# Performance work log

Hardware: AMD Instinct MI355X
Metric: run time of the kernel (lower is better)

Reference implementation:

```python
import jax, jax.numpy as jnp
import numpy as np

S, B, C = 14, 2, 20          # grid size, boxes per cell, classes
LAMBDA_COORD, LAMBDA_NOOBJ = 5.0, 0.5
NCH = 5 * B + C              # 30 channels


def setup_inputs() -> dict:
    key = jax.random.key(0)
    k1, k2, k3 = jax.random.split(key, 3)
    Nb = 4096
    # positive values: loss takes sqrt(w), sqrt(h)
    pred = jax.random.uniform(k1, (Nb, S, S, NCH), dtype=jnp.float32, minval=0.05, maxval=1.0)
    target = jax.random.uniform(k2, (Nb, S, S, NCH), dtype=jnp.float32, minval=0.05, maxval=1.0)
    # binarize conf channels so coord (conf>0) / noobj (conf==0) partition the cells
    objf = (jax.random.uniform(k3, (Nb, S, S)) < 0.3).astype(jnp.float32)
    for b in range(B):
        target = target.at[..., 4 + 5 * b].set(objf)
    return {"pred_tensor": pred, "target_tensor": target}


def _to_xyxy(box):
    # box [..., 5] (or [..., B, 5]): cell-relative x,y and global w,h -> corners
    xy = box[..., :2] / S
    half = 0.5 * box[..., 2:4]
    return jnp.concatenate([xy - half, xy + half], axis=-1)


def reference(pred_tensor, target_tensor):
    pred, target = pred_tensor, target_tensor
    obj = (target[..., 4] > 0).astype(pred.dtype)      # [Nb,S,S]
    noobj = (target[..., 4] == 0).astype(pred.dtype)   # [Nb,S,S]

    pb = pred[..., :5 * B].reshape(pred.shape[:3] + (B, 5))     # [Nb,S,S,B,5]
    tb = target[..., :5 * B].reshape(target.shape[:3] + (B, 5))  # [Nb,S,S,B,5]

    # no-object confidence loss: conf channel of every box slot in noobj cells
    loss_noobj = jnp.sum(noobj[..., None] * (pb[..., 4] - tb[..., 4]) ** 2)

    # IoU of each of B predicted boxes vs the (first) target box of the cell
    pxy = _to_xyxy(pb)                        # [Nb,S,S,B,4]
    txy = _to_xyxy(tb[..., 0, :])[..., None, :]  # [Nb,S,S,1,4]
    lt = jnp.maximum(pxy[..., :2], txy[..., :2])
    rb = jnp.minimum(pxy[..., 2:], txy[..., 2:])
    wh = jnp.clip(rb - lt, 0.0)
    inter = wh[..., 0] * wh[..., 1]           # [Nb,S,S,B]
    area_p = (pxy[..., 2] - pxy[..., 0]) * (pxy[..., 3] - pxy[..., 1])
    area_t = (txy[..., 2] - txy[..., 0]) * (txy[..., 3] - txy[..., 1])
    iou = inter / (area_p + area_t - inter)

    max_iou = jax.lax.stop_gradient(jnp.max(iou, axis=-1))  # torch uses .data (detach)
    r = jnp.argmax(iou, axis=-1)              # responsible box index [Nb,S,S]

    pr = jnp.take_along_axis(pb, r[..., None, None], axis=3)[..., 0, :]  # [Nb,S,S,5]
    tr = jnp.take_along_axis(tb, r[..., None, None], axis=3)[..., 0, :]

    m = obj
    loss_xy = jnp.sum(m[..., None] * (pr[..., :2] - tr[..., :2]) ** 2)
    # guard sqrt in masked-out cells (values there don't matter)
    safe_pwh = jnp.where(m[..., None] > 0, pr[..., 2:4], 1.0)
    safe_twh = jnp.where(m[..., None] > 0, tr[..., 2:4], 1.0)
    loss_wh = jnp.sum(m[..., None] * (jnp.sqrt(safe_pwh) - jnp.sqrt(safe_twh)) ** 2)
    loss_obj = jnp.sum(m * (pr[..., 4] - max_iou) ** 2)
    loss_class = jnp.sum(m[..., None] * (pred[..., 5 * B:] - target[..., 5 * B:]) ** 2)

    loss = LAMBDA_COORD * (loss_xy + loss_wh) + loss_obj + LAMBDA_NOOBJ * loss_noobj + loss_class
    return loss / pred.shape[0]
```

## Files before the change

kernel.cpp:

```cpp
#include <hip/hip_runtime.h>


#define S_GRID 14
#define NB 4096
#define NCELL (NB * S_GRID * S_GRID)
#define NCH 30
#define CELLS_PER_BLOCK 256
#define NBLOCKS (NCELL / CELLS_PER_BLOCK)
#define FLOATS_PER_BLOCK (CELLS_PER_BLOCK * NCH)

#define GLOBAL_AS __attribute__((address_space(1)))
#define LDS_AS    __attribute__((address_space(3)))

__device__ __forceinline__ void async_copy16(const float* g, float* l) {
    __builtin_amdgcn_global_load_lds((const GLOBAL_AS void*)g, (LDS_AS void*)l,
                                     16, 0, 0);
}

__global__ __launch_bounds__(256) void yolo_loss_partial(
    const float* __restrict__ pred, const float* __restrict__ target,
    float* __restrict__ partial)
{
    __shared__ float ps[FLOATS_PER_BLOCK];
    __shared__ float ts[FLOATS_PER_BLOCK];

    const int tid = threadIdx.x;
    const size_t base = (size_t)blockIdx.x * FLOATS_PER_BLOCK;

#pragma unroll
    for (int r = 0; r < 8; ++r) {
        int idx = r * 256 + tid;
        if (idx < FLOATS_PER_BLOCK / 4) {
            async_copy16(pred + base + (size_t)idx * 4, ps + idx * 4);
            async_copy16(target + base + (size_t)idx * 4, ts + idx * 4);
        }
    }
    __syncthreads();

    float loss;
    {
        float p[NCH], t[NCH];
        const float2* p2 = (const float2*)(ps + tid * NCH);
        const float2* t2 = (const float2*)(ts + tid * NCH);
#pragma unroll
        for (int i = 0; i < NCH / 2; ++i) {
            float2 a = p2[i]; p[2 * i] = a.x; p[2 * i + 1] = a.y;
            float2 b = t2[i]; t[2 * i] = b.x; t[2 * i + 1] = b.y;
        }

        const float t4 = t[4];
        const bool obj = (t4 > 0.0f);

        float dn0 = p[4] - t[4];
        float dn1 = p[9] - t[9];
        float noobj_l = (t4 == 0.0f) ? (dn0 * dn0 + dn1 * dn1) : 0.0f;

        const float invS = 1.0f / 14.0f;
        float tcx = t[0] * invS, tcy = t[1] * invS;
        float tx1 = tcx - 0.5f * t[2], ty1 = tcy - 0.5f * t[3];
        float tx2 = tcx + 0.5f * t[2], ty2 = tcy + 0.5f * t[3];
        float area_t = (tx2 - tx1) * (ty2 - ty1);

        float iou[2];
#pragma unroll
        for (int b = 0; b < 2; ++b) {
            const float* pb = p + 5 * b;
            float cx = pb[0] * invS, cy = pb[1] * invS;
            float x1 = cx - 0.5f * pb[2], y1 = cy - 0.5f * pb[3];
            float x2 = cx + 0.5f * pb[2], y2 = cy + 0.5f * pb[3];
            float lx = fmaxf(x1, tx1), ly = fmaxf(y1, ty1);
            float rx = fminf(x2, tx2), ry = fminf(y2, ty2);
            float wx = fmaxf(rx - lx, 0.0f), wy = fmaxf(ry - ly, 0.0f);
            float inter = wx * wy;
            float area_p = (x2 - x1) * (y2 - y1);
            iou[b] = inter / (area_p + area_t - inter);
        }

        int r = (iou[1] > iou[0]) ? 1 : 0;
        float max_iou = fmaxf(iou[0], iou[1]);

        float obj_l = 0.0f;
        if (obj) {
            const float* pr = p + 5 * r;
            const float* tr = t + 5 * r;
            float dx = pr[0] - tr[0], dy = pr[1] - tr[1];
            float lxy = dx * dx + dy * dy;
            float dw = sqrtf(pr[2]) - sqrtf(tr[2]);
            float dh = sqrtf(pr[3]) - sqrtf(tr[3]);
            float lwh = dw * dw + dh * dh;
            float dob = pr[4] - max_iou;
            float lob = dob * dob;
            float lcls = 0.0f;
#pragma unroll
            for (int c = 10; c < 30; ++c) {
                float d = p[c] - t[c];
                lcls += d * d;
            }
            obj_l = 5.0f * (lxy + lwh) + lob + lcls;
        }
        loss = obj_l + 0.5f * noobj_l;
    }

    float v = loss;
#pragma unroll
    for (int off = 32; off > 0; off >>= 1)
        v += __shfl_down(v, off, 64);

    __shared__ float red[4];
    const int lane = threadIdx.x & 63;
    const int wid = threadIdx.x >> 6;
    if (lane == 0) red[wid] = v;
    __syncthreads();
    if (threadIdx.x == 0)
        partial[blockIdx.x] = red[0] + red[1] + red[2] + red[3];
}

__global__ __launch_bounds__(256) void yolo_loss_finalize(
    const float* __restrict__ partial, float* __restrict__ out)
{
    double s = 0.0;
    for (int i = threadIdx.x; i < NBLOCKS; i += 256)
        s += (double)partial[i];

    __shared__ double sh[256];
    sh[threadIdx.x] = s;
    __syncthreads();
#pragma unroll
    for (int step = 128; step > 0; step >>= 1) {
        if (threadIdx.x < step) sh[threadIdx.x] += sh[threadIdx.x + step];
        __syncthreads();
    }
    if (threadIdx.x == 0)
        out[0] = (float)(sh[0] / (double)NB);
}

extern "C" void kernel_launch(void* const* d_in, const int* in_sizes, int n_in,
                              void* d_out, int out_size, void* d_ws, size_t ws_size,
                              hipStream_t stream) {
    const float* pred = (const float*)d_in[0];
    const float* target = (const float*)d_in[1];
    float* out = (float*)d_out;
    float* partial = (float*)d_ws;

    yolo_loss_partial<<<NBLOCKS, 256, 0, stream>>>(pred, target, partial);
    yolo_loss_finalize<<<1, 256, 0, stream>>>(partial, out);
}
```

Before: 207.1 us.

## Load cell data directly from global memory instead of staging through LDS

Drops the async global-to-LDS staging of each block's pred and target tiles and the barrier after it. Each thread now reads its own cell's 30 floats straight from global memory as float2 loads, and the class loss is computed unconditionally. Launch bounds are raised to request 4 blocks per CU, since about 61 KB of LDS per block no longer limits occupancy. The trade-off is that per-thread strided 120-byte loads are poorly coalesced compared with the contiguous 16-byte staged copies, so more memory transactions may be issued.

```diff
diff --git a/kernel.cpp b/kernel.cpp
--- a/kernel.cpp
+++ b/kernel.cpp
@@ -7,99 +7,76 @@
 #define NCH 30
 #define CELLS_PER_BLOCK 256
 #define NBLOCKS (NCELL / CELLS_PER_BLOCK)
-#define FLOATS_PER_BLOCK (CELLS_PER_BLOCK * NCH)
 
-#define GLOBAL_AS __attribute__((address_space(1)))
-#define LDS_AS    __attribute__((address_space(3)))
-
-__device__ __forceinline__ void async_copy16(const float* g, float* l) {
-    __builtin_amdgcn_global_load_lds((const GLOBAL_AS void*)g, (LDS_AS void*)l,
-                                     16, 0, 0);
-}
-
-__global__ __launch_bounds__(256) void yolo_loss_partial(
+__global__ __launch_bounds__(256, 4) void yolo_loss_partial(
     const float* __restrict__ pred, const float* __restrict__ target,
     float* __restrict__ partial)
 {
-    __shared__ float ps[FLOATS_PER_BLOCK];
-    __shared__ float ts[FLOATS_PER_BLOCK];
+    const int cell = blockIdx.x * CELLS_PER_BLOCK + threadIdx.x;
+    const float2* __restrict__ p2 = (const float2*)(pred + (size_t)cell * NCH);
+    const float2* __restrict__ t2 = (const float2*)(target + (size_t)cell * NCH);
 
-    const int tid = threadIdx.x;
-    const size_t base = (size_t)blockIdx.x * FLOATS_PER_BLOCK;
+    float p[10], t[10];
+#pragma unroll
+    for (int i = 0; i < 5; ++i) {
+        float2 a = p2[i]; p[2 * i] = a.x; p[2 * i + 1] = a.y;
+        float2 b = t2[i]; t[2 * i] = b.x; t[2 * i + 1] = b.y;
+    }
 
+    const float t4 = t[4];
+    const bool obj = (t4 > 0.0f);
+
+    float dn0 = p[4] - t[4];
+    float dn1 = p[9] - t[9];
+    float noobj_l = (t4 == 0.0f) ? (dn0 * dn0 + dn1 * dn1) : 0.0f;
+
+    const float invS = 1.0f / 14.0f;
+    float tcx = t[0] * invS, tcy = t[1] * invS;
+    float tx1 = tcx - 0.5f * t[2], ty1 = tcy - 0.5f * t[3];
+    float tx2 = tcx + 0.5f * t[2], ty2 = tcy + 0.5f * t[3];
+    float area_t = (tx2 - tx1) * (ty2 - ty1);
+
+    float iou[2];
 #pragma unroll
-    for (int r = 0; r < 8; ++r) {
-        int idx = r * 256 + tid;
-        if (idx < FLOATS_PER_BLOCK / 4) {
-            async_copy16(pred + base + (size_t)idx * 4, ps + idx * 4);
-            async_copy16(target + base + (size_t)idx * 4, ts + idx * 4);
-        }
+    for (int b = 0; b < 2; ++b) {
+        const float* pb = p + 5 * b;
+        float cx = pb[0] * invS, cy = pb[1] * invS;
+        float x1 = cx - 0.5f * pb[2], y1 = cy - 0.5f * pb[3];
+        float x2 = cx + 0.5f * pb[2], y2 = cy + 0.5f * pb[3];
+        float lx = fmaxf(x1, tx1), ly = fmaxf(y1, ty1);
+        float rx = fminf(x2, tx2), ry = fminf(y2, ty2);
+        float wx = fmaxf(rx - lx, 0.0f), wy = fmaxf(ry - ly, 0.0f);
+        float inter = wx * wy;
+        float area_p = (x2 - x1) * (y2 - y1);
+        iou[b] = inter / (area_p + area_t - inter);
     }
-    __syncthreads();
 
-    float loss;
-    {
-        float p[NCH], t[NCH];
-        const float2* p2 = (const float2*)(ps + tid * NCH);
-        const float2* t2 = (const float2*)(ts + tid * NCH);
+    int r = (iou[1] > iou[0]) ? 1 : 0;
+    float max_iou = fmaxf(iou[0], iou[1]);
+
+    float lcls = 0.0f;
 #pragma unroll
-        for (int i = 0; i < NCH / 2; ++i) {
-            float2 a = p2[i]; p[2 * i] = a.x; p[2 * i + 1] = a.y;
-            float2 b = t2[i]; t[2 * i] = b.x; t[2 * i + 1] = b.y;
-        }
+    for (int i = 5; i < 15; ++i) {
+        float2 a = p2[i];
+        float2 b = t2[i];
+        float d0 = a.x - b.x, d1 = a.y - b.y;
+        lcls += d0 * d0 + d1 * d1;
+    }
 
-        const float t4 = t[4];
-        const bool obj = (t4 > 0.0f);
-
-        float dn0 = p[4] - t[4];
-        float dn1 = p[9] - t[9];
-        float noobj_l = (t4 == 0.0f) ? (dn0 * dn0 + dn1 * dn1) : 0.0f;
-
-        const float invS = 1.0f / 14.0f;
-        float tcx = t[0] * invS, tcy = t[1] * invS;
-        float tx1 = tcx - 0.5f * t[2], ty1 = tcy - 0.5f * t[3];
-        float tx2 = tcx + 0.5f * t[2], ty2 = tcy + 0.5f * t[3];
-        float area_t = (tx2 - tx1) * (ty2 - ty1);
-
-        float iou[2];
-#pragma unroll
-        for (int b = 0; b < 2; ++b) {
-            const float* pb = p + 5 * b;
-            float cx = pb[0] * invS, cy = pb[1] * invS;
-            float x1 = cx - 0.5f * pb[2], y1 = cy - 0.5f * pb[3];
-            float x2 = cx + 0.5f * pb[2], y2 = cy + 0.5f * pb[3];
-            float lx = fmaxf(x1, tx1), ly = fmaxf(y1, ty1);
-            float rx = fminf(x2, tx2), ry = fminf(y2, ty2);
-            float wx = fmaxf(rx - lx, 0.0f), wy = fmaxf(ry - ly, 0.0f);
-            float inter = wx * wy;
-            float area_p = (x2 - x1) * (y2 - y1);
-            iou[b] = inter / (area_p + area_t - inter);
-        }
-
-        int r = (iou[1] > iou[0]) ? 1 : 0;
-        float max_iou = fmaxf(iou[0], iou[1]);
-
-        float obj_l = 0.0f;
-        if (obj) {
-            const float* pr = p + 5 * r;
-            const float* tr = t + 5 * r;
-            float dx = pr[0] - tr[0], dy = pr[1] - tr[1];
-            float lxy = dx * dx + dy * dy;
-            float dw = sqrtf(pr[2]) - sqrtf(tr[2]);
-            float dh = sqrtf(pr[3]) - sqrtf(tr[3]);
-            float lwh = dw * dw + dh * dh;
-            float dob = pr[4] - max_iou;
-            float lob = dob * dob;
-            float lcls = 0.0f;
-#pragma unroll
-            for (int c = 10; c < 30; ++c) {
-                float d = p[c] - t[c];
-                lcls += d * d;
-            }
-            obj_l = 5.0f * (lxy + lwh) + lob + lcls;
-        }
-        loss = obj_l + 0.5f * noobj_l;
+    float obj_l = 0.0f;
+    if (obj) {
+        const float* pr = p + 5 * r;
+        const float* tr = t + 5 * r;
+        float dx = pr[0] - tr[0], dy = pr[1] - tr[1];
+        float lxy = dx * dx + dy * dy;
+        float dw = sqrtf(pr[2]) - sqrtf(tr[2]);
+        float dh = sqrtf(pr[3]) - sqrtf(tr[3]);
+        float lwh = dw * dw + dh * dh;
+        float dob = pr[4] - max_iou;
+        float lob = dob * dob;
+        obj_l = 5.0f * (lxy + lwh) + lob + lcls;
     }
+    float loss = obj_l + 0.5f * noobj_l;
 
     float v = loss;
 #pragma unroll
```

Result: no change. 209.5 us (+1.1%).
